# Optimization experiments

Measured on AMD Instinct MI355X. Metric: run time of the kernel, lower is better.

## Reference

```python
import jax, jax.numpy as jnp
import numpy as np

B, D1, D2, D3 = 4, 64, 64, 64
CIN, COUT = 32, 32
M1, M2, M3 = 8, 8, 8


def setup_inputs() -> dict:
    key = jax.random.key(0)
    k1, k2, k3 = jax.random.split(key, 3)
    x = jax.random.normal(k1, (B, D1, D2, D3, CIN), dtype=jnp.float32)
    # scale ~ random_normal initializer (stddev 0.05 default in keras)
    w_real = jax.random.normal(k2, (CIN, COUT, M1, M2, M3), dtype=jnp.float32) * 0.05
    w_imag = jax.random.normal(k3, (CIN, COUT, M1, M2, M3), dtype=jnp.float32) * 0.05
    return {"x": x, "w_real": w_real, "w_imag": w_imag}


def reference(x, w_real, w_imag):
    # tf.signal.fft3d transforms the innermost 3 dims of [B,D1,D2,D3,C]
    x_ft = jnp.fft.fftn(x.astype(jnp.complex64), axes=(2, 3, 4))
    # low-mode truncation over axes 1,2,3 (as in the original code)
    x_low = x_ft[:, :M1, :M2, :M3, :]                       # [B,M1,M2,M3,CIN]
    w = (w_real + 1j * w_imag).astype(jnp.complex64)         # [CIN,COUT,M1,M2,M3]
    x_low = jnp.transpose(x_low, (0, 4, 1, 2, 3))            # [B,CIN,M1,M2,M3]
    # Faithful to original: i,j of weights are summed out, k is matched.
    out_low = jnp.einsum('bcmnk,coijk->bomnk', x_low, w)     # [B,COUT,M1,M2,M3]
    out_low = jnp.transpose(out_low, (0, 2, 3, 4, 1))        # [B,M1,M2,M3,COUT]
    # zero-padded spectrum (replaces the wasteful tensor_scatter_nd_update)
    out_ft = jnp.zeros((B, D1, D2, D3, COUT), dtype=jnp.complex64)
    out_ft = out_ft.at[:, :M1, :M2, :M3, :].set(out_low)
    y = jnp.fft.ifftn(out_ft, axes=(2, 3, 4))
    return jnp.real(y).astype(jnp.float32)
```

## Files before the change

### kernel.cpp

```cpp
#include <hip/hip_runtime.h>


#define PI2F 6.28318530717958647692f

typedef float vf4 __attribute__((ext_vector_type(4)));

__device__ __forceinline__ float2 cmul(float2 a, float2 b) {
    return make_float2(a.x * b.x - a.y * b.y, a.x * b.y + a.y * b.x);
}

__global__ void k_weff(const float* __restrict__ wr, const float* __restrict__ wi,
                       float2* __restrict__ Weff) {
    int t = blockIdx.x * 256 + threadIdx.x;
    int base = (t >> 3) * 512 + (t & 7);
    float sr = 0.f, si = 0.f;
    #pragma unroll 8
    for (int ij = 0; ij < 64; ++ij) { sr += wr[base + ij * 8]; si += wi[base + ij * 8]; }
    Weff[t] = make_float2(sr, si);
}

__global__ void k_T(const float2* __restrict__ Weff, float2* __restrict__ T) {
    __shared__ float2 tw32[32];
    __shared__ float2 A[256];
    int t = threadIdx.x;
    int c = blockIdx.x;
    if (t < 32) {
        float s, co_;
        __sincosf((PI2F / 32.f) * (float)t, &s, &co_);
        tw32[t] = make_float2(co_, s);
    }
    __syncthreads();
    {
        float2 acc = make_float2(0.f, 0.f);
        for (int fc = 0; fc < 32; ++fc) {
            float2 v = Weff[fc * 256 + t];
            float2 e = tw32[(fc * c) & 31];
            acc.x += v.x * e.x + v.y * e.y;
            acc.y += v.y * e.x - v.x * e.y;
        }
        A[t] = acc;
    }
    __syncthreads();
    {
        int f3 = t >> 5, co = t & 31;
        float2 acc = make_float2(0.f, 0.f);
        for (int o = 0; o < 32; ++o) {
            float2 v = A[o * 8 + f3];
            float2 e = tw32[(o * co) & 31];
            acc.x += v.x * e.x - v.y * e.y;
            acc.y += v.x * e.y + v.y * e.x;
        }
        T[c * 256 + t] = acc;
    }
}

__global__ void k_mid2(const float* __restrict__ x, const float2* __restrict__ T,
                       float2* __restrict__ S6) {
    __shared__ float2 lin[2048];
    __shared__ float2 ls2[256];
    __shared__ float2 ls5[256];
    __shared__ float2 tw64[64];
    int t = threadIdx.x;
    int gid = blockIdx.x;
    int f2 = gid >> 5;
    int s  = gid & 31;
    int b  = s >> 3, d1 = s & 7;
    if (t < 64) {
        float sn, cs;
        __sincosf((PI2F / 64.f) * (float)t, &sn, &cs);
        tw64[t] = make_float2(cs, sn);
    }
    {
        int c4 = t & 7;
        int d3a = t >> 3;
        const float4* pa = (const float4*)(x + (size_t)b * 8388608 + (size_t)d1 * 131072
                                             + d3a * 32 + c4 * 4);
        const float4* pb = pa + 256;
        float sn, cs;
        __sincosf((PI2F / 64.f) * (float)f2, &sn, &cs);
        float2 step = make_float2(cs, -sn);
        float2 w = make_float2(1.f, 0.f);
        float2 accA0 = {0,0}, accA1 = {0,0}, accA2 = {0,0}, accA3 = {0,0};
        float2 accB0 = {0,0}, accB1 = {0,0}, accB2 = {0,0}, accB3 = {0,0};
        #pragma unroll 4
        for (int d2 = 0; d2 < 64; ++d2) {
            float4 va = pa[d2 * 512];
            float4 vb = pb[d2 * 512];
            accA0.x += va.x * w.x; accA0.y += va.x * w.y;
            accA1.x += va.y * w.x; accA1.y += va.y * w.y;
            accA2.x += va.z * w.x; accA2.y += va.z * w.y;
            accA3.x += va.w * w.x; accA3.y += va.w * w.y;
            accB0.x += vb.x * w.x; accB0.y += vb.x * w.y;
            accB1.x += vb.y * w.x; accB1.y += vb.y * w.y;
            accB2.x += vb.z * w.x; accB2.y += vb.z * w.y;
            accB3.x += vb.w * w.x; accB3.y += vb.w * w.y;
            w = cmul(w, step);
        }
        float2* la = lin + d3a * 32 + c4 * 4;
        float2* lb = la + 1024;
        la[0] = accA0; la[1] = accA1; la[2] = accA2; la[3] = accA3;
        lb[0] = accB0; lb[1] = accB1; lb[2] = accB2; lb[3] = accB3;
    }
    __syncthreads();
    {
        int f3 = t >> 5, c = t & 31;
        float2 e = tw64[f3];
        float2 step = make_float2(e.x, -e.y);
        float2 w = make_float2(1.f, 0.f);
        float2 acc = make_float2(0.f, 0.f);
        for (int d3 = 0; d3 < 64; ++d3) {
            float2 v = lin[d3 * 32 + c];
            acc.x += v.x * w.x - v.y * w.y;
            acc.y += v.x * w.y + v.y * w.x;
            w = cmul(w, step);
        }
        ls2[f3 * 32 + c] = acc;
    }
    __syncthreads();
    {
        int f3 = t >> 5;
        float2 acc = make_float2(0.f, 0.f);
        for (int c = 0; c < 32; ++c) {
            float2 a = ls2[f3 * 32 + c];
            float2 w = T[c * 256 + t];
            acc.x += a.x * w.x - a.y * w.y;
            acc.y += a.x * w.y + a.y * w.x;
        }
        ls5[t] = acc;
    }
    __syncthreads();
    {
        int co = t & 31, d3r = t >> 5;
        float2* outp = S6 + (size_t)(s * 8 + f2) * 2048;
        #pragma unroll
        for (int j = 0; j < 8; ++j) {
            int d3 = d3r + 8 * j;
            float2 acc = make_float2(0.f, 0.f);
            #pragma unroll
            for (int f3 = 0; f3 < 8; ++f3) {
                float2 v = ls5[f3 * 32 + co];
                float2 e = tw64[(f3 * d3) & 63];
                acc.x += v.x * e.x - v.y * e.y;
                acc.y += v.x * e.y + v.y * e.x;
            }
            outp[d3 * 32 + co] = acc;
        }
    }
}

__global__ void k_final2(const float2* __restrict__ S6, float* __restrict__ out) {
    __shared__ float2 ls[2048];
    __shared__ float2 tw[64];
    int t = threadIdx.x;
    int gid = blockIdx.x;
    int blk = gid & 7;
    int d1  = (gid >> 3) & 63;
    int b   = gid >> 9;
    int co4 = t & 7;
    int d3r = (t >> 3) & 7;
    int d2q = t >> 6;
    float* obase = out + (size_t)b * 8388608 + (size_t)d1 * 131072
                 + (blk * 8 + d3r) * 32 + co4 * 4;
    if (d1 >= 8) {
        vf4 z = {0.f, 0.f, 0.f, 0.f};
        #pragma unroll
        for (int i = 0; i < 16; ++i) {
            int d2 = d2q * 16 + i;
            __builtin_nontemporal_store(z, (vf4*)(obase + d2 * 2048));
        }
        return;
    }
    if (t < 64) {
        float sn, cs;
        __sincosf((PI2F / 64.f) * (float)t, &sn, &cs);
        tw[t] = make_float2(cs, sn);
    }
    {
        const float4* src = (const float4*)(S6 + (size_t)(b * 8 + d1) * 16384);
        float4* dst = (float4*)ls;
        #pragma unroll
        for (int j = 0; j < 4; ++j) {
            int i4 = t + j * 256;
            int f2 = i4 >> 7, rem = i4 & 127;
            dst[i4] = src[f2 * 1024 + blk * 128 + rem];
        }
    }
    __syncthreads();
    float2 v[8][4];
    #pragma unroll
    for (int f2 = 0; f2 < 8; ++f2) {
        #pragma unroll
        for (int k = 0; k < 4; ++k)
            v[f2][k] = ls[f2 * 256 + d3r * 32 + co4 * 4 + k];
    }
    const float sc = 1.f / 131072.f;
    #pragma unroll 2
    for (int i = 0; i < 16; ++i) {
        int d2 = d2q * 16 + i;
        float rx = 0.f, ry = 0.f, rz = 0.f, rw = 0.f;
        #pragma unroll
        for (int f2 = 0; f2 < 8; ++f2) {
            float2 e = tw[(f2 * d2) & 63];
            rx += v[f2][0].x * e.x - v[f2][0].y * e.y;
            ry += v[f2][1].x * e.x - v[f2][1].y * e.y;
            rz += v[f2][2].x * e.x - v[f2][2].y * e.y;
            rw += v[f2][3].x * e.x - v[f2][3].y * e.y;
        }
        vf4 r = {rx * sc, ry * sc, rz * sc, rw * sc};
        __builtin_nontemporal_store(r, (vf4*)(obase + d2 * 2048));
    }
}

extern "C" void kernel_launch(void* const* d_in, const int* in_sizes, int n_in,
                              void* d_out, int out_size, void* d_ws, size_t ws_size,
                              hipStream_t stream) {
    const float* x  = (const float*)d_in[0];
    const float* wr = (const float*)d_in[1];
    const float* wi = (const float*)d_in[2];
    float* out = (float*)d_out;

    float2* Weff = (float2*)d_ws;
    float2* T    = Weff + 8192;
    float2* S6   = T + 8192;

    k_weff  <<<32,   256, 0, stream>>>(wr, wi, Weff);
    k_T     <<<32,   256, 0, stream>>>(Weff, T);
    k_mid2  <<<256,  256, 0, stream>>>(x, T, S6);
    k_final2<<<2048, 256, 0, stream>>>(S6, out);
}
```

Baseline: 241.3 us.

## Split forward DFT into separate kernel and parallelize reductions across more threads

The old k_mid2 fused the d2 DFT over x with later stages, which left it only 256 blocks that each looped serially over 64 d2 rows. That DFT now runs in a new k_dft2 kernel of 2048 blocks, each doing partial sums through shared memory, and writes an intermediate S1 buffer. k_weff, k_T and a new k_mid3 spread their reduction loops over more threads or larger blocks and combine the partial sums in LDS. The aim is better occupancy and latency hiding, paid for by an extra kernel launch and a round trip of about 4 MB through global memory for S1.

```diff
diff --git a/kernel.cpp b/kernel.cpp
--- a/kernel.cpp
+++ b/kernel.cpp
@@ -11,16 +11,27 @@
 
 __global__ void k_weff(const float* __restrict__ wr, const float* __restrict__ wi,
                        float2* __restrict__ Weff) {
-    int t = blockIdx.x * 256 + threadIdx.x;
-    int base = (t >> 3) * 512 + (t & 7);
+    __shared__ float2 ls[256];
+    int t = threadIdx.x;
+    int eL = t & 31, ijg = t >> 5;
+    int e = blockIdx.x * 32 + eL;
+    int base = (e >> 3) * 512 + (e & 7) + ijg * 64;
     float sr = 0.f, si = 0.f;
-    #pragma unroll 8
-    for (int ij = 0; ij < 64; ++ij) { sr += wr[base + ij * 8]; si += wi[base + ij * 8]; }
-    Weff[t] = make_float2(sr, si);
+    #pragma unroll
+    for (int j = 0; j < 8; ++j) { sr += wr[base + j * 8]; si += wi[base + j * 8]; }
+    ls[t] = make_float2(sr, si);
+    __syncthreads();
+    if (t < 32) {
+        float2 a = ls[t];
+        #pragma unroll
+        for (int g = 1; g < 8; ++g) { float2 v = ls[g * 32 + t]; a.x += v.x; a.y += v.y; }
+        Weff[blockIdx.x * 32 + t] = a;
+    }
 }
 
 __global__ void k_T(const float2* __restrict__ Weff, float2* __restrict__ T) {
     __shared__ float2 tw32[32];
+    __shared__ float2 P[1024];
     __shared__ float2 A[256];
     int t = threadIdx.x;
     int c = blockIdx.x;
@@ -31,119 +42,171 @@
     }
     __syncthreads();
     {
+        int g = t >> 8, rem = t & 255;
         float2 acc = make_float2(0.f, 0.f);
-        for (int fc = 0; fc < 32; ++fc) {
-            float2 v = Weff[fc * 256 + t];
+        #pragma unroll
+        for (int k = 0; k < 8; ++k) {
+            int fc = g * 8 + k;
+            float2 v = Weff[fc * 256 + rem];
             float2 e = tw32[(fc * c) & 31];
             acc.x += v.x * e.x + v.y * e.y;
             acc.y += v.y * e.x - v.x * e.y;
         }
-        A[t] = acc;
-    }
-    __syncthreads();
-    {
-        int f3 = t >> 5, co = t & 31;
+        P[t] = acc;
+    }
+    __syncthreads();
+    if (t < 256) {
+        float2 a = P[t];
+        #pragma unroll
+        for (int g = 1; g < 4; ++g) { float2 v = P[g * 256 + t]; a.x += v.x; a.y += v.y; }
+        A[t] = a;
+    }
+    __syncthreads();
+    {
+        int g = t >> 8, rem = t & 255;
+        int f3 = rem >> 5, co = rem & 31;
         float2 acc = make_float2(0.f, 0.f);
-        for (int o = 0; o < 32; ++o) {
+        #pragma unroll
+        for (int k = 0; k < 8; ++k) {
+            int o = g * 8 + k;
             float2 v = A[o * 8 + f3];
             float2 e = tw32[(o * co) & 31];
             acc.x += v.x * e.x - v.y * e.y;
             acc.y += v.x * e.y + v.y * e.x;
         }
-        T[c * 256 + t] = acc;
-    }
-}
-
-__global__ void k_mid2(const float* __restrict__ x, const float2* __restrict__ T,
-                       float2* __restrict__ S6) {
-    __shared__ float2 lin[2048];
-    __shared__ float2 ls2[256];
-    __shared__ float2 ls5[256];
+        P[t] = acc;
+    }
+    __syncthreads();
+    if (t < 256) {
+        float2 a = P[t];
+        #pragma unroll
+        for (int g = 1; g < 4; ++g) { float2 v = P[g * 256 + t]; a.x += v.x; a.y += v.y; }
+        T[c * 256 + t] = a;
+    }
+}
+
+__global__ void k_dft2(const float* __restrict__ x, float2* __restrict__ S1) {
     __shared__ float2 tw64[64];
+    __shared__ float2 P[2048];
     int t = threadIdx.x;
     int gid = blockIdx.x;
-    int f2 = gid >> 5;
-    int s  = gid & 31;
-    int b  = s >> 3, d1 = s & 7;
+    int d3 = gid & 63, s = gid >> 6;
+    int b = s >> 3, d1 = s & 7;
+    int c = t & 31, d2g = t >> 5;
     if (t < 64) {
         float sn, cs;
         __sincosf((PI2F / 64.f) * (float)t, &sn, &cs);
         tw64[t] = make_float2(cs, sn);
     }
-    {
-        int c4 = t & 7;
-        int d3a = t >> 3;
-        const float4* pa = (const float4*)(x + (size_t)b * 8388608 + (size_t)d1 * 131072
-                                             + d3a * 32 + c4 * 4);
-        const float4* pb = pa + 256;
+    __syncthreads();
+    const float* xp = x + (size_t)b * 8388608 + (size_t)d1 * 131072 + d3 * 32 + c;
+    float2 acc[8];
+    #pragma unroll
+    for (int f2 = 0; f2 < 8; ++f2) acc[f2] = make_float2(0.f, 0.f);
+    #pragma unroll
+    for (int k = 0; k < 8; ++k) {
+        int d2 = d2g * 8 + k;
+        float v = xp[d2 * 2048];
+        #pragma unroll
+        for (int f2 = 0; f2 < 8; ++f2) {
+            float2 e = tw64[(f2 * d2) & 63];
+            acc[f2].x += v * e.x;
+            acc[f2].y -= v * e.y;
+        }
+    }
+    #pragma unroll
+    for (int f2 = 0; f2 < 8; ++f2) P[(d2g * 8 + f2) * 32 + c] = acc[f2];
+    __syncthreads();
+    {
+        int f2 = t >> 5, cc = t & 31;
+        float2 a = make_float2(0.f, 0.f);
+        #pragma unroll
+        for (int g = 0; g < 8; ++g) {
+            float2 v = P[(g * 8 + f2) * 32 + cc];
+            a.x += v.x; a.y += v.y;
+        }
+        S1[(size_t)(s * 8 + f2) * 2048 + d3 * 32 + cc] = a;
+    }
+}
+
+__global__ void k_mid3(const float2* __restrict__ S1, const float2* __restrict__ T,
+                       float2* __restrict__ S6) {
+    __shared__ float2 sl1[2048];
+    __shared__ float2 P[1024];
+    __shared__ float2 s2[256];
+    __shared__ float2 s5[256];
+    __shared__ float2 tw[64];
+    int t = threadIdx.x;
+    int gid = blockIdx.x;
+    if (t < 64) {
         float sn, cs;
-        __sincosf((PI2F / 64.f) * (float)f2, &sn, &cs);
-        float2 step = make_float2(cs, -sn);
-        float2 w = make_float2(1.f, 0.f);
-        float2 accA0 = {0,0}, accA1 = {0,0}, accA2 = {0,0}, accA3 = {0,0};
-        float2 accB0 = {0,0}, accB1 = {0,0}, accB2 = {0,0}, accB3 = {0,0};
+        __sincosf((PI2F / 64.f) * (float)t, &sn, &cs);
+        tw[t] = make_float2(cs, sn);
+    }
+    {
+        const float4* src = (const float4*)(S1 + (size_t)gid * 2048);
+        ((float4*)sl1)[t] = src[t];
+    }
+    __syncthreads();
+    {
+        int g = t >> 8, rem = t & 255;
+        int f3 = rem >> 5, c = rem & 31;
+        float2 a = make_float2(0.f, 0.f);
         #pragma unroll 4
-        for (int d2 = 0; d2 < 64; ++d2) {
-            float4 va = pa[d2 * 512];
-            float4 vb = pb[d2 * 512];
-            accA0.x += va.x * w.x; accA0.y += va.x * w.y;
-            accA1.x += va.y * w.x; accA1.y += va.y * w.y;
-            accA2.x += va.z * w.x; accA2.y += va.z * w.y;
-            accA3.x += va.w * w.x; accA3.y += va.w * w.y;
-            accB0.x += vb.x * w.x; accB0.y += vb.x * w.y;
-            accB1.x += vb.y * w.x; accB1.y += vb.y * w.y;
-            accB2.x += vb.z * w.x; accB2.y += vb.z * w.y;
-            accB3.x += vb.w * w.x; accB3.y += vb.w * w.y;
-            w = cmul(w, step);
-        }
-        float2* la = lin + d3a * 32 + c4 * 4;
-        float2* lb = la + 1024;
-        la[0] = accA0; la[1] = accA1; la[2] = accA2; la[3] = accA3;
-        lb[0] = accB0; lb[1] = accB1; lb[2] = accB2; lb[3] = accB3;
-    }
-    __syncthreads();
-    {
-        int f3 = t >> 5, c = t & 31;
-        float2 e = tw64[f3];
-        float2 step = make_float2(e.x, -e.y);
-        float2 w = make_float2(1.f, 0.f);
-        float2 acc = make_float2(0.f, 0.f);
-        for (int d3 = 0; d3 < 64; ++d3) {
-            float2 v = lin[d3 * 32 + c];
-            acc.x += v.x * w.x - v.y * w.y;
-            acc.y += v.x * w.y + v.y * w.x;
-            w = cmul(w, step);
-        }
-        ls2[f3 * 32 + c] = acc;
-    }
-    __syncthreads();
-    {
-        int f3 = t >> 5;
-        float2 acc = make_float2(0.f, 0.f);
-        for (int c = 0; c < 32; ++c) {
-            float2 a = ls2[f3 * 32 + c];
-            float2 w = T[c * 256 + t];
-            acc.x += a.x * w.x - a.y * w.y;
-            acc.y += a.x * w.y + a.y * w.x;
-        }
-        ls5[t] = acc;
-    }
-    __syncthreads();
-    {
-        int co = t & 31, d3r = t >> 5;
-        float2* outp = S6 + (size_t)(s * 8 + f2) * 2048;
-        #pragma unroll
-        for (int j = 0; j < 8; ++j) {
-            int d3 = d3r + 8 * j;
-            float2 acc = make_float2(0.f, 0.f);
+        for (int k = 0; k < 16; ++k) {
+            int d3 = g * 16 + k;
+            float2 v = sl1[d3 * 32 + c];
+            float2 e = tw[(f3 * d3) & 63];
+            a.x += v.x * e.x + v.y * e.y;
+            a.y += v.y * e.x - v.x * e.y;
+        }
+        P[t] = a;
+    }
+    __syncthreads();
+    if (t < 256) {
+        float2 a = P[t];
+        #pragma unroll
+        for (int g = 1; g < 4; ++g) { float2 v = P[g * 256 + t]; a.x += v.x; a.y += v.y; }
+        s2[t] = a;
+    }
+    __syncthreads();
+    {
+        int g = t >> 8, rem = t & 255;
+        int f3 = rem >> 5, co = rem & 31;
+        float2 a = make_float2(0.f, 0.f);
+        #pragma unroll
+        for (int k = 0; k < 8; ++k) {
+            int cc = g * 8 + k;
+            float2 v = s2[f3 * 32 + cc];
+            float2 w = T[cc * 256 + f3 * 32 + co];
+            a.x += v.x * w.x - v.y * w.y;
+            a.y += v.x * w.y + v.y * w.x;
+        }
+        P[t] = a;
+    }
+    __syncthreads();
+    if (t < 256) {
+        float2 a = P[t];
+        #pragma unroll
+        for (int g = 1; g < 4; ++g) { float2 v = P[g * 256 + t]; a.x += v.x; a.y += v.y; }
+        s5[t] = a;
+    }
+    __syncthreads();
+    {
+        int co = t & 31, d3a = t >> 5;
+        float2* outp = S6 + (size_t)gid * 2048;
+        #pragma unroll
+        for (int h = 0; h < 2; ++h) {
+            int d3 = d3a + 32 * h;
+            float2 a = make_float2(0.f, 0.f);
             #pragma unroll
             for (int f3 = 0; f3 < 8; ++f3) {
-                float2 v = ls5[f3 * 32 + co];
-                float2 e = tw64[(f3 * d3) & 63];
-                acc.x += v.x * e.x - v.y * e.y;
-                acc.y += v.x * e.y + v.y * e.x;
+                float2 v = s5[f3 * 32 + co];
+                float2 e = tw[(f3 * d3) & 63];
+                a.x += v.x * e.x - v.y * e.y;
+                a.y += v.x * e.y + v.y * e.x;
             }
-            outp[d3 * 32 + co] = acc;
+            outp[d3 * 32 + co] = a;
         }
     }
 }
@@ -221,10 +284,12 @@
 
     float2* Weff = (float2*)d_ws;
     float2* T    = Weff + 8192;
-    float2* S6   = T + 8192;
-
-    k_weff  <<<32,   256, 0, stream>>>(wr, wi, Weff);
-    k_T     <<<32,   256, 0, stream>>>(Weff, T);
-    k_mid2  <<<256,  256, 0, stream>>>(x, T, S6);
-    k_final2<<<2048, 256, 0, stream>>>(S6, out);
-}
+    float2* S1   = T + 8192;
+    float2* S6   = S1 + 524288;
+
+    k_weff  <<<256,  256,  0, stream>>>(wr, wi, Weff);
+    k_T     <<<32,   1024, 0, stream>>>(Weff, T);
+    k_dft2  <<<2048, 256,  0, stream>>>(x, S1);
+    k_mid3  <<<256,  1024, 0, stream>>>(S1, T, S6);
+    k_final2<<<2048, 256,  0, stream>>>(S6, out);
+}
```

Result: faster. 222.9 us (-7.6%).
